# Kernel optimization log

Hardware: AMD Instinct MI355X
Metric: run time of the kernel (lower is better)

The kernel has to match this reference:

```python
import jax, jax.numpy as jnp
import numpy as np

H_HEADS = 8
DIM_HEAD = 64
NEG_BIAS = -1.0e9


def setup_inputs() -> dict:
    key = jax.random.key(0)
    ks = jax.random.split(key, 8)
    b, n, l = 4, 4096, 256
    qd, cd = 512, 768
    inner = H_HEADS * DIM_HEAD  # 512
    x = jax.random.normal(ks[0], (b, n, qd), dtype=jnp.float32)
    context = jax.random.normal(ks[1], (b, l, cd), dtype=jnp.float32)
    mask = jax.random.randint(ks[2], (b, l, 128, 128), 0, 2).astype(jnp.int32)
    Wq = jax.random.normal(ks[3], (qd, inner), dtype=jnp.float32) * 0.02
    Wk = jax.random.normal(ks[4], (cd, inner), dtype=jnp.float32) * 0.02
    Wv = jax.random.normal(ks[5], (cd, inner), dtype=jnp.float32) * 0.02
    Wo = jax.random.normal(ks[6], (inner, qd), dtype=jnp.float32) * 0.02
    bo = jnp.zeros((qd,), dtype=jnp.float32)
    return {"x": x, "context": context, "mask": mask,
            "Wq": Wq, "Wk": Wk, "Wv": Wv, "Wo": Wo, "bo": bo}


def _split_heads(t, h):
    # 'b n (h d) -> (b h) n d'
    b, n, hd = t.shape
    d = hd // h
    return t.reshape(b, n, h, d).transpose(0, 2, 1, 3).reshape(b * h, n, d)


def reference(x, context, mask, Wq, Wk, Wv, Wo, bo):
    h = H_HEADS
    scale = DIM_HEAD ** (-0.5)
    b, n, _ = x.shape
    l = context.shape[1]
    size = int(round(n ** 0.5))  # spatial side of the query grid

    q = _split_heads(x @ Wq, h)        # (b*h, n, d)
    k = _split_heads(context @ Wk, h)  # (b*h, l, d)
    v = _split_heads(context @ Wv, h)  # (b*h, l, d)

    sim = jnp.einsum('bid,bjd->bij', q, k) * scale  # (b*h, n, l)

    # F.interpolate(mask, size=size) with default 'nearest': idx = floor(i * H_in / size)
    Hin = mask.shape[2]
    idx = (jnp.arange(size) * Hin) // size
    m = mask[:, :, idx[:, None], idx[None, :]]       # (b, l, size, size)
    m = m.reshape(b, l, n).transpose(0, 2, 1)        # (b, n, l)
    m = jnp.tile(m, (h, 1, 1)).astype(bool)          # (b*h, n, l), tile order as in torch .tile(h,1,1)
    sim = jnp.where(m, sim, sim + NEG_BIAS)

    attn = jax.nn.softmax(sim, axis=-1)
    out = jnp.einsum('bij,bjd->bid', attn, v)        # (b*h, n, d)
    # '(b h) n d -> b n (h d)'
    out = out.reshape(b, h, n, DIM_HEAD).transpose(0, 2, 1, 3).reshape(b, n, h * DIM_HEAD)
    return out @ Wo + bo
```

## Files before the change

### kernel.cpp

```cpp
#include <hip/hip_runtime.h>

typedef __attribute__((ext_vector_type(8))) short short8;
typedef __attribute__((ext_vector_type(4))) float f32x4;

__device__ __forceinline__ unsigned short f2bf(float f) {
  unsigned int u = __float_as_uint(f);
  u = (u + 0x7FFFu + ((u >> 16) & 1u)) >> 16;
  return (unsigned short)u;
}

__device__ __forceinline__ void gl_lds16(const void* g, void* l) {
  __builtin_amdgcn_global_load_lds(
      (const __attribute__((address_space(1))) void*)g,
      (__attribute__((address_space(3))) void*)l, 16, 0, 0);
}

__global__ void cvt_both(const float* __restrict__ x, const float* __restrict__ ctx,
                         unsigned short* __restrict__ xb, unsigned short* __restrict__ ctxb) {
  int i = blockIdx.x * 256 + threadIdx.x;
  const float4* src;
  ushort4* dst;
  if (i < 2097152) {
    src = (const float4*)x + i;
    dst = (ushort4*)xb + i;
  } else {
    int j = i - 2097152;
    if (j >= 196608) return;
    src = (const float4*)ctx + j;
    dst = (ushort4*)ctxb + j;
  }
  float4 v = *src;
  ushort4 o;
  o.x = f2bf(v.x); o.y = f2bf(v.y); o.z = f2bf(v.z); o.w = f2bf(v.w);
  *dst = o;
}

__global__ void prep_all(const float* __restrict__ Wq, const float* __restrict__ Wk,
                         const float* __restrict__ Wv, const float* __restrict__ Wo,
                         unsigned short* __restrict__ WqT, unsigned short* __restrict__ WkT,
                         unsigned short* __restrict__ WvT, unsigned short* __restrict__ WoT,
                         const int* __restrict__ mask, unsigned char* __restrict__ Mout) {
  __shared__ char smem[64 * 256];
  const int bid = blockIdx.x;
  if (bid < 320) {
    unsigned short(*t)[65] = (unsigned short(*)[65])smem;
    const float* W; unsigned short* WT; int K, rel;
    if (bid < 64)       { W = Wq; WT = WqT; K = 512; rel = bid; }
    else if (bid < 160) { W = Wk; WT = WkT; K = 768; rel = bid - 64; }
    else if (bid < 256) { W = Wv; WT = WvT; K = 768; rel = bid - 160; }
    else                { W = Wo; WT = WoT; K = 512; rel = bid - 256; }
    const int N = 512;
    const int tk = rel >> 3, tn = rel & 7;
    const int k0 = tk * 64, n0 = tn * 64;
    const int tt = threadIdx.x;
#pragma unroll
    for (int e = 0; e < 16; ++e) {
      int idx = e * 256 + tt;
      int r = idx >> 6, c = idx & 63;
      t[r][c] = f2bf(W[(size_t)(k0 + r) * N + n0 + c]);
    }
    __syncthreads();
#pragma unroll
    for (int e = 0; e < 16; ++e) {
      int idx = e * 256 + tt;
      int rr = idx & 63, cc = idx >> 6;
      WT[(size_t)(n0 + cc) * K + k0 + rr] = t[rr][cc];
    }
  } else {
    unsigned char* bits = (unsigned char*)smem;
    const int rel = bid - 320;
    const int r2g = rel & 63, bp = rel >> 6;
    const int j = threadIdx.x;
    const int4* row = (const int4*)(mask + ((size_t)(bp * 256 + j) * 128 + r2g * 2) * 128);
#pragma unroll 8
    for (int q = 0; q < 32; ++q) {
      int4 v = row[q];
      bits[(2 * q) * 256 + j] = v.x ? 1 : 0;
      bits[(2 * q + 1) * 256 + j] = v.z ? 1 : 0;
    }
    __syncthreads();
    const int t2 = threadIdx.x;
    const int c = t2 >> 2, ch = t2 & 3;
    uint4* dst = (uint4*)(Mout + ((size_t)bp * 4096 + r2g * 64 + c) * 256 + ch * 64);
#pragma unroll
    for (int q = 0; q < 4; ++q) {
      unsigned int wd[4];
#pragma unroll
      for (int wq = 0; wq < 4; ++wq) {
        unsigned int v = 0;
#pragma unroll
        for (int bb = 0; bb < 4; ++bb) {
          int ob = ch * 64 + q * 16 + wq * 4 + bb;
          int jj = ((ob & 15) << 4) | (ob >> 4);
          v |= ((unsigned int)bits[c * 256 + jj]) << (8 * bb);
        }
        wd[wq] = v;
      }
      uint4 vv; vv.x = wd[0]; vv.y = wd[1]; vv.z = wd[2]; vv.w = wd[3];
      dst[q] = vv;
    }
  }
}

template <int MODE>
__global__ void gemm128(const unsigned short* __restrict__ A,
                        const unsigned short* __restrict__ BT,
                        void* __restrict__ Cout, const float* __restrict__ bias,
                        int M, int N, int K) {
  __shared__ unsigned short lds_a[128 * 64];
  __shared__ unsigned short lds_b[128 * 64];
  const int tid = threadIdx.x;
  const int w = tid >> 6, lane = tid & 63;
  const int lo = lane & 15, hi = lane >> 4;
  const int bid = blockIdx.x;
  const int chunk = gridDim.x >> 3;
  const int wg = (bid & 7) * chunk + (bid >> 3);
  const int tN = N >> 7;
  const int m0 = (wg / tN) * 128, n0 = (wg % tN) * 128;
  const int wr = w >> 1, wc = w & 1;
  f32x4 acc[4][4];
#pragma unroll
  for (int m = 0; m < 4; ++m)
#pragma unroll
    for (int n = 0; n < 4; ++n) acc[m][n] = (f32x4){0.f, 0.f, 0.f, 0.f};

  for (int k0 = 0; k0 < K; k0 += 64) {
    __syncthreads();
#pragma unroll
    for (int c = 0; c < 4; ++c) {
      int o = (tid + c * 256) * 16;
      int row = o >> 7, colb = o & 127;
      gl_lds16((const char*)A + ((size_t)(m0 + row) * K + k0) * 2 + colb,
               (char*)lds_a + (w * 64 + c * 256) * 16);
    }
#pragma unroll
    for (int c = 0; c < 4; ++c) {
      int o = (tid + c * 256) * 16;
      int row = o >> 7, colb = o & 127;
      gl_lds16((const char*)BT + ((size_t)(n0 + row) * K + k0) * 2 + colb,
               (char*)lds_b + (w * 64 + c * 256) * 16);
    }
    __syncthreads();
    short8 a[2][4], b[2][4];
#pragma unroll
    for (int kk = 0; kk < 2; ++kk) {
#pragma unroll
      for (int m = 0; m < 4; ++m)
        a[kk][m] = *(const short8*)&lds_a[(wr * 64 + m * 16 + lo) * 64 + kk * 32 + hi * 8];
#pragma unroll
      for (int n = 0; n < 4; ++n)
        b[kk][n] = *(const short8*)&lds_b[(wc * 64 + n * 16 + lo) * 64 + kk * 32 + hi * 8];
    }
#pragma unroll
    for (int kk = 0; kk < 2; ++kk)
#pragma unroll
      for (int m = 0; m < 4; ++m)
#pragma unroll
        for (int n = 0; n < 4; ++n)
          acc[m][n] = __builtin_amdgcn_mfma_f32_16x16x32_bf16(a[kk][m], b[kk][n], acc[m][n], 0, 0, 0);
  }

#pragma unroll
  for (int m = 0; m < 4; ++m)
#pragma unroll
    for (int n = 0; n < 4; ++n) {
      int rbase = m0 + wr * 64 + m * 16 + hi * 4;
      int col = n0 + wc * 64 + n * 16 + lo;
#pragma unroll
      for (int r = 0; r < 4; ++r) {
        int rowg = rbase + r;
        float v = acc[m][n][r];
        if (MODE == 0) {
          ((unsigned short*)Cout)[(size_t)rowg * N + col] = f2bf(v);
        } else {
          ((float*)Cout)[(size_t)rowg * N + col] = v + bias[col];
        }
      }
    }
}

__global__ void gemm_kv64(const unsigned short* __restrict__ A,
                          const unsigned short* __restrict__ WkT,
                          const unsigned short* __restrict__ WvT,
                          unsigned short* __restrict__ Kb, unsigned short* __restrict__ VTb) {
  __shared__ unsigned short la[64 * 64];
  __shared__ unsigned short lb[64 * 64];
  const int z = blockIdx.z;
  const unsigned short* BT = z ? WvT : WkT;
  const int tid = threadIdx.x;
  const int w = tid >> 6, lane = tid & 63;
  const int lo = lane & 15, hi = lane >> 4;
  const int m0 = blockIdx.x * 64, n0 = blockIdx.y * 64;
  const int wr = w >> 1, wc = w & 1;
  const int K = 768;
  f32x4 acc[2][2];
#pragma unroll
  for (int m = 0; m < 2; ++m)
#pragma unroll
    for (int n = 0; n < 2; ++n) acc[m][n] = (f32x4){0.f, 0.f, 0.f, 0.f};

  for (int k0 = 0; k0 < K; k0 += 64) {
    __syncthreads();
#pragma unroll
    for (int c = 0; c < 2; ++c) {
      int o = (tid + c * 256) * 16;
      int row = o >> 7, colb = o & 127;
      gl_lds16((const char*)A + ((size_t)(m0 + row) * K + k0) * 2 + colb,
               (char*)la + (w * 64 + c * 256) * 16);
      gl_lds16((const char*)BT + ((size_t)(n0 + row) * K + k0) * 2 + colb,
               (char*)lb + (w * 64 + c * 256) * 16);
    }
    __syncthreads();
    short8 a[2][2], b[2][2];
#pragma unroll
    for (int kk = 0; kk < 2; ++kk) {
#pragma unroll
      for (int m = 0; m < 2; ++m)
        a[kk][m] = *(const short8*)&la[(wr * 32 + m * 16 + lo) * 64 + kk * 32 + hi * 8];
#pragma unroll
      for (int n = 0; n < 2; ++n)
        b[kk][n] = *(const short8*)&lb[(wc * 32 + n * 16 + lo) * 64 + kk * 32 + hi * 8];
    }
#pragma unroll
    for (int kk = 0; kk < 2; ++kk)
#pragma unroll
      for (int m = 0; m < 2; ++m)
#pragma unroll
        for (int n = 0; n < 2; ++n)
          acc[m][n] = __builtin_amdgcn_mfma_f32_16x16x32_bf16(a[kk][m], b[kk][n], acc[m][n], 0, 0, 0);
  }

#pragma unroll
  for (int m = 0; m < 2; ++m)
#pragma unroll
    for (int n = 0; n < 2; ++n) {
      int col = n0 + wc * 32 + n * 16 + lo;
#pragma unroll
      for (int r = 0; r < 4; ++r) {
        int rowg = m0 + wr * 32 + m * 16 + hi * 4 + r;
        unsigned short v = f2bf(acc[m][n][r]);
        if (z == 0)
          Kb[(size_t)rowg * 512 + col] = v;
        else
          VTb[((size_t)(rowg >> 8) * 512 + col) * 256 + (rowg & 255)] = v;
      }
    }
}

__global__ void attn_kernel(const unsigned short* __restrict__ Qb,
                            const unsigned short* __restrict__ Kb,
                            const unsigned short* __restrict__ VTb,
                            const unsigned char* __restrict__ Mu8,
                            unsigned short* __restrict__ AOb) {
  __shared__ unsigned short kt[256 * 64];
  const int tid = threadIdx.x, w = tid >> 6, lane = tid & 63;
  const int lo = lane & 15, hi = lane >> 4;
  const int bid = blockIdx.x;
  const int wg = (bid & 7) * 256 + (bid >> 3);
  const int qt = wg & 63, h = (wg >> 6) & 7, b = wg >> 9;

#pragma unroll
  for (int c = 0; c < 8; ++c) {
    int o = (tid + c * 256) * 16;
    int j = o >> 7, colb = (o & 127) ^ ((j & 7) << 4);
    gl_lds16((const char*)Kb + ((size_t)((b * 256 + j) * 512 + h * 64)) * 2 + colb,
             (char*)kt + (w * 64 + c * 256) * 16);
  }
  short8 qf[2];
  {
    int qrow = qt * 64 + w * 16 + lo;
#pragma unroll
    for (int kk = 0; kk < 2; ++kk)
      qf[kk] = *(const short8*)&Qb[(size_t)(b * 4096 + qrow) * 512 + h * 64 + kk * 32 + hi * 8];
  }
  __syncthreads();

  f32x4 acc[16];
#pragma unroll
  for (int nt = 0; nt < 16; ++nt) acc[nt] = (f32x4){0.f, 0.f, 0.f, 0.f};
  __builtin_amdgcn_s_setprio(1);
#pragma unroll
  for (int nt = 0; nt < 16; ++nt) {
    int j = nt * 16 + lo;
#pragma unroll
    for (int kk = 0; kk < 2; ++kk) {
      short8 bfr = *(const short8*)((const char*)kt + j * 128 +
                                    (((kk * 32 + hi * 8) * 2) ^ ((j & 7) << 4)));
      acc[nt] = __builtin_amdgcn_mfma_f32_16x16x32_bf16(qf[kk], bfr, acc[nt], 0, 0, 0);
    }
  }
  __builtin_amdgcn_s_setprio(0);

  const unsigned char* mrow = Mu8 + ((size_t)(h & 3) * 4096 + qt * 64 + w * 16) * 256;
  uint4 mv[4];
#pragma unroll
  for (int r = 0; r < 4; ++r)
    mv[r] = *(const uint4*)(mrow + (hi * 4 + r) * 256 + lo * 16);

  float rmax[4] = {-3e38f, -3e38f, -3e38f, -3e38f};
#pragma unroll
  for (int nt = 0; nt < 16; ++nt)
#pragma unroll
    for (int r = 0; r < 4; ++r) {
      float s = acc[nt][r] * 0.125f;
      acc[nt][r] = s;
      rmax[r] = fmaxf(rmax[r], s);
    }
#pragma unroll
  for (int r = 0; r < 4; ++r) {
#pragma unroll
    for (int m2 = 1; m2 < 16; m2 <<= 1)
      rmax[r] = fmaxf(rmax[r], __shfl_xor(rmax[r], m2, 64));
  }
  float rsum[4] = {0.f, 0.f, 0.f, 0.f};
#pragma unroll
  for (int nt = 0; nt < 16; ++nt)
#pragma unroll
    for (int r = 0; r < 4; ++r) {
      unsigned int word = (nt < 4) ? mv[r].x : (nt < 8) ? mv[r].y : (nt < 12) ? mv[r].z : mv[r].w;
      unsigned int mbyte = (word >> ((nt & 3) * 8)) & 0xFFu;
      float p = __expf(acc[nt][r] - rmax[r]);
      p = mbyte ? p : 0.f;
      acc[nt][r] = p;
      rsum[r] += p;
    }
#pragma unroll
  for (int r = 0; r < 4; ++r) {
#pragma unroll
    for (int m2 = 1; m2 < 16; m2 <<= 1)
      rsum[r] += __shfl_xor(rsum[r], m2, 64);
    rsum[r] = 1.f / rsum[r];
  }

  __syncthreads();

  {
    unsigned short* pl = kt;
#pragma unroll
    for (int r = 0; r < 4; ++r) {
      int q = w * 16 + hi * 4 + r;
      char* prow = (char*)pl + q * 512;
      int q7s = (q & 7) << 4;
#pragma unroll
      for (int nt = 0; nt < 16; ++nt) {
        *(unsigned short*)(prow + (((nt * 16 + lo) * 2) ^ q7s)) = f2bf(acc[nt][r] * rsum[r]);
      }
    }
  }
  __syncthreads();

  const int dh = w & 1, qh = w >> 1;
  f32x4 aco[2][2];
#pragma unroll
  for (int m = 0; m < 2; ++m)
#pragma unroll
    for (int n = 0; n < 2; ++n) aco[m][n] = (f32x4){0.f, 0.f, 0.f, 0.f};
  const size_t vbase = ((size_t)b * 512 + h * 64 + dh * 32) * 256;
#pragma unroll
  for (int ks = 0; ks < 8; ++ks) {
    short8 pa[2];
#pragma unroll
    for (int m = 0; m < 2; ++m) {
      int q = qh * 32 + m * 16 + lo;
      pa[m] = *(const short8*)((const char*)kt + q * 512 +
                               (((ks * 32 + hi * 8) * 2) ^ ((q & 7) << 4)));
    }
    __builtin_amdgcn_s_setprio(1);
#pragma unroll
    for (int n = 0; n < 2; ++n) {
      short8 vb = *(const short8*)&VTb[vbase + (size_t)(n * 16 + lo) * 256 + ks * 32 + hi * 8];
#pragma unroll
      for (int m = 0; m < 2; ++m)
        aco[m][n] = __builtin_amdgcn_mfma_f32_16x16x32_bf16(pa[m], vb, aco[m][n], 0, 0, 0);
    }
    __builtin_amdgcn_s_setprio(0);
  }

#pragma unroll
  for (int m = 0; m < 2; ++m)
#pragma unroll
    for (int n = 0; n < 2; ++n) {
      int col = h * 64 + dh * 32 + n * 16 + lo;
#pragma unroll
      for (int r = 0; r < 4; ++r) {
        int rowg = qt * 64 + qh * 32 + m * 16 + hi * 4 + r;
        AOb[(size_t)(b * 4096 + rowg) * 512 + col] = f2bf(aco[m][n][r]);
      }
    }
}

extern "C" void kernel_launch(void* const* d_in, const int* in_sizes, int n_in,
                              void* d_out, int out_size, void* d_ws, size_t ws_size,
                              hipStream_t stream) {
  const float* x = (const float*)d_in[0];
  const float* ctx = (const float*)d_in[1];
  const int* mask = (const int*)d_in[2];
  const float* Wq = (const float*)d_in[3];
  const float* Wk = (const float*)d_in[4];
  const float* Wv = (const float*)d_in[5];
  const float* Wo = (const float*)d_in[6];
  const float* bo = (const float*)d_in[7];
  float* out = (float*)d_out;

  char* ws = (char*)d_ws;
  size_t off = 0;
  auto alloc = [&](size_t bytes) {
    char* p = ws + off;
    off += (bytes + 255) & ~(size_t)255;
    return p;
  };
  unsigned short* xb   = (unsigned short*)alloc((size_t)16384 * 512 * 2);
  unsigned short* ctxb = (unsigned short*)alloc((size_t)1024 * 768 * 2);
  unsigned short* WqT  = (unsigned short*)alloc((size_t)512 * 512 * 2);
  unsigned short* WkT  = (unsigned short*)alloc((size_t)512 * 768 * 2);
  unsigned short* WvT  = (unsigned short*)alloc((size_t)512 * 768 * 2);
  unsigned short* WoT  = (unsigned short*)alloc((size_t)512 * 512 * 2);
  unsigned short* Qb   = (unsigned short*)alloc((size_t)16384 * 512 * 2);
  unsigned short* Kb   = (unsigned short*)alloc((size_t)1024 * 512 * 2);
  unsigned short* VTb  = (unsigned short*)alloc((size_t)4 * 512 * 256 * 2);
  unsigned short* AOb  = (unsigned short*)alloc((size_t)16384 * 512 * 2);
  unsigned char*  Mu8  = (unsigned char*)alloc((size_t)4 * 4096 * 256);

  cvt_both<<<8960, 256, 0, stream>>>(x, ctx, xb, ctxb);
  prep_all<<<576, 256, 0, stream>>>(Wq, Wk, Wv, Wo, WqT, WkT, WvT, WoT, mask, Mu8);

  gemm_kv64<<<dim3(16, 8, 2), 256, 0, stream>>>(ctxb, WkT, WvT, Kb, VTb);
  gemm128<0><<<512, 256, 0, stream>>>(xb, WqT, Qb, nullptr, 16384, 512, 512);

  attn_kernel<<<2048, 256, 0, stream>>>(Qb, Kb, VTb, Mu8, AOb);

  gemm128<2><<<512, 256, 0, stream>>>(AOb, WoT, out, bo, 16384, 512, 512);
}
```

Measured before the change: 100.2 us.

## Merge prep/convert and Q/K/V projection launches; fold softmax scale and normalization

Merges the fp32-to-bf16 conversion into the weight/mask prep kernel, and the Q and K/V projections into one launch, cutting the kernel count from six to four. The 1/sqrt(d) scale is folded into Wq during weight prep, so the attention kernel no longer multiplies each score. Softmax normalization is deferred to the output, scaling the 64-wide PV result instead of each 256-wide probability row. The mask load is hoisted ahead of the QK MFMA loop. Folding the scale into bf16 Wq changes rounding slightly, and merged launches mix heterogeneous block workloads.

Measured after the change: 102.0 us. No clear change (+1.8%).

```diff
diff --git a/kernel.cpp b/kernel.cpp
--- a/kernel.cpp
+++ b/kernel.cpp
@@ -15,37 +15,39 @@
       (__attribute__((address_space(3))) void*)l, 16, 0, 0);
 }
 
-__global__ void cvt_both(const float* __restrict__ x, const float* __restrict__ ctx,
-                         unsigned short* __restrict__ xb, unsigned short* __restrict__ ctxb) {
-  int i = blockIdx.x * 256 + threadIdx.x;
-  const float4* src;
-  ushort4* dst;
-  if (i < 2097152) {
-    src = (const float4*)x + i;
-    dst = (ushort4*)xb + i;
-  } else {
-    int j = i - 2097152;
-    if (j >= 196608) return;
-    src = (const float4*)ctx + j;
-    dst = (ushort4*)ctxb + j;
-  }
-  float4 v = *src;
-  ushort4 o;
-  o.x = f2bf(v.x); o.y = f2bf(v.y); o.z = f2bf(v.z); o.w = f2bf(v.w);
-  *dst = o;
-}
-
 __global__ void prep_all(const float* __restrict__ Wq, const float* __restrict__ Wk,
                          const float* __restrict__ Wv, const float* __restrict__ Wo,
                          unsigned short* __restrict__ WqT, unsigned short* __restrict__ WkT,
                          unsigned short* __restrict__ WvT, unsigned short* __restrict__ WoT,
-                         const int* __restrict__ mask, unsigned char* __restrict__ Mout) {
+                         const int* __restrict__ mask, unsigned char* __restrict__ Mout,
+                         const float* __restrict__ x, const float* __restrict__ ctx,
+                         unsigned short* __restrict__ xb, unsigned short* __restrict__ ctxb) {
   __shared__ char smem[64 * 256];
   const int bid = blockIdx.x;
+  if (bid >= 576) {
+    int i = (bid - 576) * 256 + threadIdx.x;
+    const float4* src;
+    ushort4* dst;
+    if (i < 2097152) {
+      src = (const float4*)x + i;
+      dst = (ushort4*)xb + i;
+    } else {
+      int j = i - 2097152;
+      if (j >= 196608) return;
+      src = (const float4*)ctx + j;
+      dst = (ushort4*)ctxb + j;
+    }
+    float4 v = *src;
+    ushort4 o;
+    o.x = f2bf(v.x); o.y = f2bf(v.y); o.z = f2bf(v.z); o.w = f2bf(v.w);
+    *dst = o;
+    return;
+  }
   if (bid < 320) {
     unsigned short(*t)[65] = (unsigned short(*)[65])smem;
     const float* W; unsigned short* WT; int K, rel;
-    if (bid < 64)       { W = Wq; WT = WqT; K = 512; rel = bid; }
+    float scale = 1.f;
+    if (bid < 64)       { W = Wq; WT = WqT; K = 512; rel = bid; scale = 0.125f; }
     else if (bid < 160) { W = Wk; WT = WkT; K = 768; rel = bid - 64; }
     else if (bid < 256) { W = Wv; WT = WvT; K = 768; rel = bid - 160; }
     else                { W = Wo; WT = WoT; K = 512; rel = bid - 256; }
@@ -57,7 +59,7 @@
     for (int e = 0; e < 16; ++e) {
       int idx = e * 256 + tt;
       int r = idx >> 6, c = idx & 63;
-      t[r][c] = f2bf(W[(size_t)(k0 + r) * N + n0 + c]);
+      t[r][c] = f2bf(scale * W[(size_t)(k0 + r) * N + n0 + c]);
     }
     __syncthreads();
 #pragma unroll
@@ -98,6 +100,279 @@
       }
       uint4 vv; vv.x = wd[0]; vv.y = wd[1]; vv.z = wd[2]; vv.w = wd[3];
       dst[q] = vv;
+    }
+  }
+}
+
+__global__ void proj_all(const unsigned short* __restrict__ xb, const unsigned short* __restrict__ ctxb,
+                         const unsigned short* __restrict__ WqT, const unsigned short* __restrict__ WkT,
+                         const unsigned short* __restrict__ WvT,
+                         unsigned short* __restrict__ Qb, unsigned short* __restrict__ Kb,
+                         unsigned short* __restrict__ VTb) {
+  __shared__ unsigned short lds_a[128 * 64];
+  __shared__ unsigned short lds_b[128 * 64];
+  const int tid = threadIdx.x;
+  const int w = tid >> 6, lane = tid & 63;
+  const int lo = lane & 15, hi = lane >> 4;
+  const int wr = w >> 1, wc = w & 1;
+  const int bid = blockIdx.x;
+  const int wg = (bid & 7) * 96 + (bid >> 3);
+
+  if (wg < 512) {
+    const int m0 = (wg >> 2) * 128, n0 = (wg & 3) * 128;
+    const int K = 512;
+    f32x4 acc[4][4];
+#pragma unroll
+    for (int m = 0; m < 4; ++m)
+#pragma unroll
+      for (int n = 0; n < 4; ++n) acc[m][n] = (f32x4){0.f, 0.f, 0.f, 0.f};
+
+    for (int k0 = 0; k0 < K; k0 += 64) {
+      __syncthreads();
+#pragma unroll
+      for (int c = 0; c < 4; ++c) {
+        int o = (tid + c * 256) * 16;
+        int row = o >> 7, colb = o & 127;
+        gl_lds16((const char*)xb + ((size_t)(m0 + row) * K + k0) * 2 + colb,
+                 (char*)lds_a + (w * 64 + c * 256) * 16);
+      }
+#pragma unroll
+      for (int c = 0; c < 4; ++c) {
+        int o = (tid + c * 256) * 16;
+        int row = o >> 7, colb = o & 127;
+        gl_lds16((const char*)WqT + ((size_t)(n0 + row) * K + k0) * 2 + colb,
+                 (char*)lds_b + (w * 64 + c * 256) * 16);
+      }
+      __syncthreads();
+      short8 a[2][4], b[2][4];
+#pragma unroll
+      for (int kk = 0; kk < 2; ++kk) {
+#pragma unroll
+        for (int m = 0; m < 4; ++m)
+          a[kk][m] = *(const short8*)&lds_a[(wr * 64 + m * 16 + lo) * 64 + kk * 32 + hi * 8];
+#pragma unroll
+        for (int n = 0; n < 4; ++n)
+          b[kk][n] = *(const short8*)&lds_b[(wc * 64 + n * 16 + lo) * 64 + kk * 32 + hi * 8];
+      }
+#pragma unroll
+      for (int kk = 0; kk < 2; ++kk)
+#pragma unroll
+        for (int m = 0; m < 4; ++m)
+#pragma unroll
+          for (int n = 0; n < 4; ++n)
+            acc[m][n] = __builtin_amdgcn_mfma_f32_16x16x32_bf16(a[kk][m], b[kk][n], acc[m][n], 0, 0, 0);
+    }
+#pragma unroll
+    for (int m = 0; m < 4; ++m)
+#pragma unroll
+      for (int n = 0; n < 4; ++n) {
+        int rbase = m0 + wr * 64 + m * 16 + hi * 4;
+        int col = n0 + wc * 64 + n * 16 + lo;
+#pragma unroll
+        for (int r = 0; r < 4; ++r)
+          Qb[(size_t)(rbase + r) * 512 + col] = f2bf(acc[m][n][r]);
+      }
+  } else {
+    const int rel = wg - 512;
+    const int z = rel >> 7, t = rel & 127;
+    const unsigned short* BT = z ? WvT : WkT;
+    const int m0 = (t >> 3) * 64, n0 = (t & 7) * 64;
+    const int K = 768;
+    f32x4 acc[2][2];
+#pragma unroll
+    for (int m = 0; m < 2; ++m)
+#pragma unroll
+      for (int n = 0; n < 2; ++n) acc[m][n] = (f32x4){0.f, 0.f, 0.f, 0.f};
+
+    for (int k0 = 0; k0 < K; k0 += 64) {
+      __syncthreads();
+#pragma unroll
+      for (int c = 0; c < 2; ++c) {
+        int o = (tid + c * 256) * 16;
+        int row = o >> 7, colb = o & 127;
+        gl_lds16((const char*)ctxb + ((size_t)(m0 + row) * K + k0) * 2 + colb,
+                 (char*)lds_a + (w * 64 + c * 256) * 16);
+        gl_lds16((const char*)BT + ((size_t)(n0 + row) * K + k0) * 2 + colb,
+                 (char*)lds_b + (w * 64 + c * 256) * 16);
+      }
+      __syncthreads();
+      short8 a[2][2], b[2][2];
+#pragma unroll
+      for (int kk = 0; kk < 2; ++kk) {
+#pragma unroll
+        for (int m = 0; m < 2; ++m)
+          a[kk][m] = *(const short8*)&lds_a[(wr * 32 + m * 16 + lo) * 64 + kk * 32 + hi * 8];
+#pragma unroll
+        for (int n = 0; n < 2; ++n)
+          b[kk][n] = *(const short8*)&lds_b[(wc * 32 + n * 16 + lo) * 64 + kk * 32 + hi * 8];
+      }
+#pragma unroll
+      for (int kk = 0; kk < 2; ++kk)
+#pragma unroll
+        for (int m = 0; m < 2; ++m)
+#pragma unroll
+          for (int n = 0; n < 2; ++n)
+            acc[m][n] = __builtin_amdgcn_mfma_f32_16x16x32_bf16(a[kk][m], b[kk][n], acc[m][n], 0, 0, 0);
+    }
+#pragma unroll
+    for (int m = 0; m < 2; ++m)
+#pragma unroll
+      for (int n = 0; n < 2; ++n) {
+        int col = n0 + wc * 32 + n * 16 + lo;
+#pragma unroll
+        for (int r = 0; r < 4; ++r) {
+          int rowg = m0 + wr * 32 + m * 16 + hi * 4 + r;
+          unsigned short v = f2bf(acc[m][n][r]);
+          if (z == 0)
+            Kb[(size_t)rowg * 512 + col] = v;
+          else
+            VTb[((size_t)(rowg >> 8) * 512 + col) * 256 + (rowg & 255)] = v;
+        }
+      }
+  }
+}
+
+__global__ void attn_kernel(const unsigned short* __restrict__ Qb,
+                            const unsigned short* __restrict__ Kb,
+                            const unsigned short* __restrict__ VTb,
+                            const unsigned char* __restrict__ Mu8,
+                            unsigned short* __restrict__ AOb) {
+  __shared__ unsigned short kt[256 * 64];
+  __shared__ float rinv_s[64];
+  const int tid = threadIdx.x, w = tid >> 6, lane = tid & 63;
+  const int lo = lane & 15, hi = lane >> 4;
+  const int bid = blockIdx.x;
+  const int wg = (bid & 7) * 256 + (bid >> 3);
+  const int qt = wg & 63, h = (wg >> 6) & 7, b = wg >> 9;
+
+#pragma unroll
+  for (int c = 0; c < 8; ++c) {
+    int o = (tid + c * 256) * 16;
+    int j = o >> 7, colb = (o & 127) ^ ((j & 7) << 4);
+    gl_lds16((const char*)Kb + ((size_t)((b * 256 + j) * 512 + h * 64)) * 2 + colb,
+             (char*)kt + (w * 64 + c * 256) * 16);
+  }
+  short8 qf[2];
+  {
+    int qrow = qt * 64 + w * 16 + lo;
+#pragma unroll
+    for (int kk = 0; kk < 2; ++kk)
+      qf[kk] = *(const short8*)&Qb[(size_t)(b * 4096 + qrow) * 512 + h * 64 + kk * 32 + hi * 8];
+  }
+  const unsigned char* mrow = Mu8 + ((size_t)(h & 3) * 4096 + qt * 64 + w * 16) * 256;
+  uint4 mv[4];
+#pragma unroll
+  for (int r = 0; r < 4; ++r)
+    mv[r] = *(const uint4*)(mrow + (hi * 4 + r) * 256 + lo * 16);
+  __syncthreads();
+
+  f32x4 acc[16];
+#pragma unroll
+  for (int nt = 0; nt < 16; ++nt) acc[nt] = (f32x4){0.f, 0.f, 0.f, 0.f};
+  __builtin_amdgcn_s_setprio(1);
+#pragma unroll
+  for (int nt = 0; nt < 16; ++nt) {
+    int j = nt * 16 + lo;
+#pragma unroll
+    for (int kk = 0; kk < 2; ++kk) {
+      short8 bfr = *(const short8*)((const char*)kt + j * 128 +
+                                    (((kk * 32 + hi * 8) * 2) ^ ((j & 7) << 4)));
+      acc[nt] = __builtin_amdgcn_mfma_f32_16x16x32_bf16(qf[kk], bfr, acc[nt], 0, 0, 0);
+    }
+  }
+  __builtin_amdgcn_s_setprio(0);
+
+  float rmax[4] = {-3e38f, -3e38f, -3e38f, -3e38f};
+#pragma unroll
+  for (int nt = 0; nt < 16; ++nt)
+#pragma unroll
+    for (int r = 0; r < 4; ++r) rmax[r] = fmaxf(rmax[r], acc[nt][r]);
+#pragma unroll
+  for (int r = 0; r < 4; ++r) {
+#pragma unroll
+    for (int m2 = 1; m2 < 16; m2 <<= 1)
+      rmax[r] = fmaxf(rmax[r], __shfl_xor(rmax[r], m2, 64));
+  }
+  float rsum[4] = {0.f, 0.f, 0.f, 0.f};
+#pragma unroll
+  for (int nt = 0; nt < 16; ++nt)
+#pragma unroll
+    for (int r = 0; r < 4; ++r) {
+      unsigned int word = (nt < 4) ? mv[r].x : (nt < 8) ? mv[r].y : (nt < 12) ? mv[r].z : mv[r].w;
+      unsigned int mbyte = (word >> ((nt & 3) * 8)) & 0xFFu;
+      float p = __expf(acc[nt][r] - rmax[r]);
+      p = mbyte ? p : 0.f;
+      acc[nt][r] = p;
+      rsum[r] += p;
+    }
+#pragma unroll
+  for (int r = 0; r < 4; ++r) {
+#pragma unroll
+    for (int m2 = 1; m2 < 16; m2 <<= 1)
+      rsum[r] += __shfl_xor(rsum[r], m2, 64);
+  }
+  if (lo == 0) {
+#pragma unroll
+    for (int r = 0; r < 4; ++r) rinv_s[w * 16 + hi * 4 + r] = 1.f / rsum[r];
+  }
+
+  __syncthreads();
+
+  {
+    unsigned short* pl = kt;
+#pragma unroll
+    for (int r = 0; r < 4; ++r) {
+      int q = w * 16 + hi * 4 + r;
+      char* prow = (char*)pl + q * 512;
+      int q7s = (q & 7) << 4;
+#pragma unroll
+      for (int nt = 0; nt < 16; ++nt) {
+        *(unsigned short*)(prow + (((nt * 16 + lo) * 2) ^ q7s)) = f2bf(acc[nt][r]);
+      }
+    }
+  }
+  __syncthreads();
+
+  const int dh = w & 1, qh = w >> 1;
+  f32x4 aco[2][2];
+#pragma unroll
+  for (int m = 0; m < 2; ++m)
+#pragma unroll
+    for (int n = 0; n < 2; ++n) aco[m][n] = (f32x4){0.f, 0.f, 0.f, 0.f};
+  const size_t vbase = ((size_t)b * 512 + h * 64 + dh * 32) * 256;
+#pragma unroll
+  for (int ks = 0; ks < 8; ++ks) {
+    short8 pa[2];
+#pragma unroll
+    for (int m = 0; m < 2; ++m) {
+      int q = qh * 32 + m * 16 + lo;
+      pa[m] = *(const short8*)((const char*)kt + q * 512 +
+                               (((ks * 32 + hi * 8) * 2) ^ ((q & 7) << 4)));
+    }
+    __builtin_amdgcn_s_setprio(1);
+#pragma unroll
+    for (int n = 0; n < 2; ++n) {
+      short8 vb = *(const short8*)&VTb[vbase + (size_t)(n * 16 + lo) * 256 + ks * 32 + hi * 8];
+#pragma unroll
+      for (int m = 0; m < 2; ++m)
+        aco[m][n] = __builtin_amdgcn_mfma_f32_16x16x32_bf16(pa[m], vb, aco[m][n], 0, 0, 0);
+    }
+    __builtin_amdgcn_s_setprio(0);
+  }
+
+#pragma unroll
+  for (int m = 0; m < 2; ++m) {
+    float rv[4];
+#pragma unroll
+    for (int r = 0; r < 4; ++r) rv[r] = rinv_s[qh * 32 + m * 16 + hi * 4 + r];
+#pragma unroll
+    for (int n = 0; n < 2; ++n) {
+      int col = h * 64 + dh * 32 + n * 16 + lo;
+#pragma unroll
+      for (int r = 0; r < 4; ++r) {
+        int rowg = qt * 64 + qh * 32 + m * 16 + hi * 4 + r;
+        AOb[(size_t)(b * 4096 + rowg) * 512 + col] = f2bf(aco[m][n][r] * rv[r]);
+      }
     }
   }
 }
@@ -175,216 +450,6 @@
         } else {
           ((float*)Cout)[(size_t)rowg * N + col] = v + bias[col];
         }
-      }
-    }
-}
-
-__global__ void gemm_kv64(const unsigned short* __restrict__ A,
-                          const unsigned short* __restrict__ WkT,
-                          const unsigned short* __restrict__ WvT,
-                          unsigned short* __restrict__ Kb, unsigned short* __restrict__ VTb) {
-  __shared__ unsigned short la[64 * 64];
-  __shared__ unsigned short lb[64 * 64];
-  const int z = blockIdx.z;
-  const unsigned short* BT = z ? WvT : WkT;
-  const int tid = threadIdx.x;
-  const int w = tid >> 6, lane = tid & 63;
-  const int lo = lane & 15, hi = lane >> 4;
-  const int m0 = blockIdx.x * 64, n0 = blockIdx.y * 64;
-  const int wr = w >> 1, wc = w & 1;
-  const int K = 768;
-  f32x4 acc[2][2];
-#pragma unroll
-  for (int m = 0; m < 2; ++m)
-#pragma unroll
-    for (int n = 0; n < 2; ++n) acc[m][n] = (f32x4){0.f, 0.f, 0.f, 0.f};
-
-  for (int k0 = 0; k0 < K; k0 += 64) {
-    __syncthreads();
-#pragma unroll
-    for (int c = 0; c < 2; ++c) {
-      int o = (tid + c * 256) * 16;
-      int row = o >> 7, colb = o & 127;
-      gl_lds16((const char*)A + ((size_t)(m0 + row) * K + k0) * 2 + colb,
-               (char*)la + (w * 64 + c * 256) * 16);
-      gl_lds16((const char*)BT + ((size_t)(n0 + row) * K + k0) * 2 + colb,
-               (char*)lb + (w * 64 + c * 256) * 16);
-    }
-    __syncthreads();
-    short8 a[2][2], b[2][2];
-#pragma unroll
-    for (int kk = 0; kk < 2; ++kk) {
-#pragma unroll
-      for (int m = 0; m < 2; ++m)
-        a[kk][m] = *(const short8*)&la[(wr * 32 + m * 16 + lo) * 64 + kk * 32 + hi * 8];
-#pragma unroll
-      for (int n = 0; n < 2; ++n)
-        b[kk][n] = *(const short8*)&lb[(wc * 32 + n * 16 + lo) * 64 + kk * 32 + hi * 8];
-    }
-#pragma unroll
-    for (int kk = 0; kk < 2; ++kk)
-#pragma unroll
-      for (int m = 0; m < 2; ++m)
-#pragma unroll
-        for (int n = 0; n < 2; ++n)
-          acc[m][n] = __builtin_amdgcn_mfma_f32_16x16x32_bf16(a[kk][m], b[kk][n], acc[m][n], 0, 0, 0);
-  }
-
-#pragma unroll
-  for (int m = 0; m < 2; ++m)
-#pragma unroll
-    for (int n = 0; n < 2; ++n) {
-      int col = n0 + wc * 32 + n * 16 + lo;
-#pragma unroll
-      for (int r = 0; r < 4; ++r) {
-        int rowg = m0 + wr * 32 + m * 16 + hi * 4 + r;
-        unsigned short v = f2bf(acc[m][n][r]);
-        if (z == 0)
-          Kb[(size_t)rowg * 512 + col] = v;
-        else
-          VTb[((size_t)(rowg >> 8) * 512 + col) * 256 + (rowg & 255)] = v;
-      }
-    }
-}
-
-__global__ void attn_kernel(const unsigned short* __restrict__ Qb,
-                            const unsigned short* __restrict__ Kb,
-                            const unsigned short* __restrict__ VTb,
-                            const unsigned char* __restrict__ Mu8,
-                            unsigned short* __restrict__ AOb) {
-  __shared__ unsigned short kt[256 * 64];
-  const int tid = threadIdx.x, w = tid >> 6, lane = tid & 63;
-  const int lo = lane & 15, hi = lane >> 4;
-  const int bid = blockIdx.x;
-  const int wg = (bid & 7) * 256 + (bid >> 3);
-  const int qt = wg & 63, h = (wg >> 6) & 7, b = wg >> 9;
-
-#pragma unroll
-  for (int c = 0; c < 8; ++c) {
-    int o = (tid + c * 256) * 16;
-    int j = o >> 7, colb = (o & 127) ^ ((j & 7) << 4);
-    gl_lds16((const char*)Kb + ((size_t)((b * 256 + j) * 512 + h * 64)) * 2 + colb,
-             (char*)kt + (w * 64 + c * 256) * 16);
-  }
-  short8 qf[2];
-  {
-    int qrow = qt * 64 + w * 16 + lo;
-#pragma unroll
-    for (int kk = 0; kk < 2; ++kk)
-      qf[kk] = *(const short8*)&Qb[(size_t)(b * 4096 + qrow) * 512 + h * 64 + kk * 32 + hi * 8];
-  }
-  __syncthreads();
-
-  f32x4 acc[16];
-#pragma unroll
-  for (int nt = 0; nt < 16; ++nt) acc[nt] = (f32x4){0.f, 0.f, 0.f, 0.f};
-  __builtin_amdgcn_s_setprio(1);
-#pragma unroll
-  for (int nt = 0; nt < 16; ++nt) {
-    int j = nt * 16 + lo;
-#pragma unroll
-    for (int kk = 0; kk < 2; ++kk) {
-      short8 bfr = *(const short8*)((const char*)kt + j * 128 +
-                                    (((kk * 32 + hi * 8) * 2) ^ ((j & 7) << 4)));
-      acc[nt] = __builtin_amdgcn_mfma_f32_16x16x32_bf16(qf[kk], bfr, acc[nt], 0, 0, 0);
-    }
-  }
-  __builtin_amdgcn_s_setprio(0);
-
-  const unsigned char* mrow = Mu8 + ((size_t)(h & 3) * 4096 + qt * 64 + w * 16) * 256;
-  uint4 mv[4];
-#pragma unroll
-  for (int r = 0; r < 4; ++r)
-    mv[r] = *(const uint4*)(mrow + (hi * 4 + r) * 256 + lo * 16);
-
-  float rmax[4] = {-3e38f, -3e38f, -3e38f, -3e38f};
-#pragma unroll
-  for (int nt = 0; nt < 16; ++nt)
-#pragma unroll
-    for (int r = 0; r < 4; ++r) {
-      float s = acc[nt][r] * 0.125f;
-      acc[nt][r] = s;
-      rmax[r] = fmaxf(rmax[r], s);
-    }
-#pragma unroll
-  for (int r = 0; r < 4; ++r) {
-#pragma unroll
-    for (int m2 = 1; m2 < 16; m2 <<= 1)
-      rmax[r] = fmaxf(rmax[r], __shfl_xor(rmax[r], m2, 64));
-  }
-  float rsum[4] = {0.f, 0.f, 0.f, 0.f};
-#pragma unroll
-  for (int nt = 0; nt < 16; ++nt)
-#pragma unroll
-    for (int r = 0; r < 4; ++r) {
-      unsigned int word = (nt < 4) ? mv[r].x : (nt < 8) ? mv[r].y : (nt < 12) ? mv[r].z : mv[r].w;
-      unsigned int mbyte = (word >> ((nt & 3) * 8)) & 0xFFu;
-      float p = __expf(acc[nt][r] - rmax[r]);
-      p = mbyte ? p : 0.f;
-      acc[nt][r] = p;
-      rsum[r] += p;
-    }
-#pragma unroll
-  for (int r = 0; r < 4; ++r) {
-#pragma unroll
-    for (int m2 = 1; m2 < 16; m2 <<= 1)
-      rsum[r] += __shfl_xor(rsum[r], m2, 64);
-    rsum[r] = 1.f / rsum[r];
-  }
-
-  __syncthreads();
-
-  {
-    unsigned short* pl = kt;
-#pragma unroll
-    for (int r = 0; r < 4; ++r) {
-      int q = w * 16 + hi * 4 + r;
-      char* prow = (char*)pl + q * 512;
-      int q7s = (q & 7) << 4;
-#pragma unroll
-      for (int nt = 0; nt < 16; ++nt) {
-        *(unsigned short*)(prow + (((nt * 16 + lo) * 2) ^ q7s)) = f2bf(acc[nt][r] * rsum[r]);
-      }
-    }
-  }
-  __syncthreads();
-
-  const int dh = w & 1, qh = w >> 1;
-  f32x4 aco[2][2];
-#pragma unroll
-  for (int m = 0; m < 2; ++m)
-#pragma unroll
-    for (int n = 0; n < 2; ++n) aco[m][n] = (f32x4){0.f, 0.f, 0.f, 0.f};
-  const size_t vbase = ((size_t)b * 512 + h * 64 + dh * 32) * 256;
-#pragma unroll
-  for (int ks = 0; ks < 8; ++ks) {
-    short8 pa[2];
-#pragma unroll
-    for (int m = 0; m < 2; ++m) {
-      int q = qh * 32 + m * 16 + lo;
-      pa[m] = *(const short8*)((const char*)kt + q * 512 +
-                               (((ks * 32 + hi * 8) * 2) ^ ((q & 7) << 4)));
-    }
-    __builtin_amdgcn_s_setprio(1);
-#pragma unroll
-    for (int n = 0; n < 2; ++n) {
-      short8 vb = *(const short8*)&VTb[vbase + (size_t)(n * 16 + lo) * 256 + ks * 32 + hi * 8];
-#pragma unroll
-      for (int m = 0; m < 2; ++m)
-        aco[m][n] = __builtin_amdgcn_mfma_f32_16x16x32_bf16(pa[m], vb, aco[m][n], 0, 0, 0);
-    }
-    __builtin_amdgcn_s_setprio(0);
-  }
-
-#pragma unroll
-  for (int m = 0; m < 2; ++m)
-#pragma unroll
-    for (int n = 0; n < 2; ++n) {
-      int col = h * 64 + dh * 32 + n * 16 + lo;
-#pragma unroll
-      for (int r = 0; r < 4; ++r) {
-        int rowg = qt * 64 + qh * 32 + m * 16 + hi * 4 + r;
-        AOb[(size_t)(b * 4096 + rowg) * 512 + col] = f2bf(aco[m][n][r]);
       }
     }
 }
@@ -421,13 +486,8 @@
   unsigned short* AOb  = (unsigned short*)alloc((size_t)16384 * 512 * 2);
   unsigned char*  Mu8  = (unsigned char*)alloc((size_t)4 * 4096 * 256);
 
-  cvt_both<<<8960, 256, 0, stream>>>(x, ctx, xb, ctxb);
-  prep_all<<<576, 256, 0, stream>>>(Wq, Wk, Wv, Wo, WqT, WkT, WvT, WoT, mask, Mu8);
-
-  gemm_kv64<<<dim3(16, 8, 2), 256, 0, stream>>>(ctxb, WkT, WvT, Kb, VTb);
-  gemm128<0><<<512, 256, 0, stream>>>(xb, WqT, Qb, nullptr, 16384, 512, 512);
-
+  prep_all<<<9536, 256, 0, stream>>>(Wq, Wk, Wv, Wo, WqT, WkT, WvT, WoT, mask, Mu8, x, ctx, xb, ctxb);
+  proj_all<<<768, 256, 0, stream>>>(xb, ctxb, WqT, WkT, WvT, Qb, Kb, VTb);
   attn_kernel<<<2048, 256, 0, stream>>>(Qb, Kb, VTb, Mu8, AOb);
-
   gemm128<2><<<512, 256, 0, stream>>>(AOb, WoT, out, bo, 16384, 512, 512);
 }
```
